# Performance work log

Hardware: AMD Instinct MI355X
Metric: run time of the kernel (lower is better)

The kernel has to match this reference:

```python
import jax, jax.numpy as jnp
import numpy as np

T, B, INPUT, HIDDEN, OUTPUT = 512, 128, 256, 512, 128

def setup_inputs() -> dict:
    key = jax.random.key(0)
    k1, k2, k3 = jax.random.split(key, 3)
    fan_in = INPUT + HIDDEN
    bound = 1.0 / np.sqrt(fan_in)
    x = jax.random.normal(k1, (T, B, INPUT), dtype=jnp.float32)
    W = jax.random.uniform(k2, (HIDDEN, fan_in), minval=-bound, maxval=bound, dtype=jnp.float32)
    b = jax.random.uniform(k3, (HIDDEN,), minval=-bound, maxval=bound, dtype=jnp.float32)
    return {"x": x, "W": W, "b": b}

def reference(x, W, b):
    # W: [H, INPUT+H] (torch Linear layout); split into input and hidden parts
    Wx = W[:, :INPUT]   # [H, I]
    Wh = W[:, INPUT:]   # [H, H]
    h0 = jnp.zeros((x.shape[1], Wh.shape[0]), dtype=x.dtype)
    # precompute input projections for all steps: [T, B, H]
    xp = jnp.einsum('tbi,hi->tbh', x, Wx) + b

    def step(h, xp_t):
        h_new = jnp.tanh(xp_t + h @ Wh.T)
        return h_new, h_new

    _, Hs = jax.lax.scan(step, h0, xp)
    return jnp.concatenate([h0[None], Hs], axis=0)  # [T+1, B, H]
```

## Files before the change

### kernel.cpp

```cpp
#include <hip/hip_runtime.h>
#include <hip/hip_bf16.h>
#include <hip/hip_fp16.h>
#include <stdint.h>

#define T_STEPS 512
#define BATCH   128
#define NIN     256
#define HID     512
#define BH      (BATCH * HID)

typedef _Float16 f16x2 __attribute__((ext_vector_type(2)));
typedef unsigned int u32x4 __attribute__((ext_vector_type(4)));

__device__ __forceinline__ float fdot2u(uint32_t a, uint32_t b, float c) {
#if __has_builtin(__builtin_amdgcn_fdot2)
  return __builtin_amdgcn_fdot2(__builtin_bit_cast(f16x2, a),
                                __builtin_bit_cast(f16x2, b), c, false);
#else
  __half2 ha = __builtin_bit_cast(__half2, a);
  __half2 hb = __builtin_bit_cast(__half2, b);
  return c + __half2float(ha.x) * __half2float(hb.x)
           + __half2float(ha.y) * __half2float(hb.y);
#endif
}

__device__ __forceinline__ float dot8(uint4 w, uint4 x, float a) {
  a = fdot2u(w.x, x.x, a);
  a = fdot2u(w.y, x.y, a);
  a = fdot2u(w.z, x.z, a);
  a = fdot2u(w.w, x.w, a);
  return a;
}

template <int CTRL>
__device__ __forceinline__ float dppadd(float v) {
  int x = __builtin_bit_cast(int, v);
  int y = __builtin_amdgcn_update_dpp(x, x, CTRL, 0xF, 0xF, true);
  return v + __builtin_bit_cast(float, y);
}
__device__ __forceinline__ float red8(float v) {
  v = dppadd<0xB1>(v);
  v = dppadd<0x4E>(v);
  v = dppadd<0x141>(v);
  return v;
}

__global__ void prep_w(const float* __restrict__ W,
                       __half* __restrict__ Wx, __half* __restrict__ Wh,
                       float* __restrict__ io) {
  int idx = blockIdx.x * 256 + threadIdx.x;
  if (idx < BH) io[idx] = 0.f;
  int h = idx / (NIN + HID);
  int c = idx - h * (NIN + HID);
  float v = W[idx];
  if (c < NIN) Wx[h * NIN + c] = __float2half(v);
  else         Wh[h * HID + (c - NIN)] = __float2half(v);
}

__launch_bounds__(256)
__global__ void gemm_xp(const float* __restrict__ x,
                        const __half* __restrict__ Wx,
                        const float* __restrict__ bias,
                        float* __restrict__ xp) {
  __shared__ __align__(16) __half xs[32][256];

  const int bid = blockIdx.x;
  const int m0 = (bid >> 1) * 32;
  const int n0 = (bid & 1) * 256;
  const int tid = threadIdx.x;

  {
    int r = tid >> 3, cb = (tid & 7) * 32;
    const float* src = x + (size_t)(m0 + r) * NIN + cb;
    union { __half h[8]; uint4 u; } cv;
#pragma unroll
    for (int i = 0; i < 4; ++i) {
      float4 f0 = *(const float4*)(src + i * 8);
      float4 f1 = *(const float4*)(src + i * 8 + 4);
      cv.h[0] = __float2half(f0.x); cv.h[1] = __float2half(f0.y);
      cv.h[2] = __float2half(f0.z); cv.h[3] = __float2half(f0.w);
      cv.h[4] = __float2half(f1.x); cv.h[5] = __float2half(f1.y);
      cv.h[6] = __float2half(f1.z); cv.h[7] = __float2half(f1.w);
      *(uint4*)(void*)&xs[r][cb + i * 8] = cv.u;
    }
  }
  __syncthreads();

  const int rg = tid >> 6;
  const int c0 = tid & 63;

  float acc[8][4];
#pragma unroll
  for (int r = 0; r < 8; ++r)
#pragma unroll
    for (int j = 0; j < 4; ++j) acc[r][j] = 0.f;

  for (int kc = 0; kc < NIN; kc += 32) {
    uint4 w[4][4];
#pragma unroll
    for (int j = 0; j < 4; ++j) {
      const __half* wp = Wx + (size_t)(n0 + c0 + 64 * j) * NIN + kc;
#pragma unroll
      for (int i = 0; i < 4; ++i) w[j][i] = *(const uint4*)(wp + i * 8);
    }
#pragma unroll
    for (int r = 0; r < 8; ++r) {
      uint4 xv[4];
#pragma unroll
      for (int i = 0; i < 4; ++i)
        xv[i] = *(const uint4*)(const void*)&xs[rg * 8 + r][kc + i * 8];
#pragma unroll
      for (int j = 0; j < 4; ++j)
#pragma unroll
        for (int i = 0; i < 4; ++i) acc[r][j] = dot8(w[j][i], xv[i], acc[r][j]);
    }
  }

  float bj[4];
#pragma unroll
  for (int j = 0; j < 4; ++j) bj[j] = bias[n0 + c0 + 64 * j];
#pragma unroll
  for (int r = 0; r < 8; ++r) {
    float* dst = xp + (size_t)(m0 + rg * 8 + r) * HID + n0 + c0;
#pragma unroll
    for (int j = 0; j < 4; ++j) dst[64 * j] = acc[r][j] + bj[j];
  }
}

#define HCH 72
__global__ __launch_bounds__(512)
__attribute__((amdgpu_waves_per_eu(2, 2)))
void rnn_scan(const __half* __restrict__ Wh, float* io) {
  __shared__ __align__(16) __half hA[8 * HCH];
  __shared__ __align__(16) __half hB[8 * HCH];

  const int bid  = blockIdx.x;
  const int b    = bid >> 1;
  const int half = bid & 1;
  const int ph0  = (1 - half) * 256;
  const int tid  = threadIdx.x;
  const int ks   = tid & 7;
  const int rb   = tid >> 3;
  const bool em  = (ks < 4);

  uint32_t w[4][32];
  {
    const __half* wrow = Wh + (size_t)(half * 256 + rb * 4) * HID + ks * 64;
#pragma unroll
    for (int r = 0; r < 4; ++r)
#pragma unroll
      for (int i = 0; i < 8; ++i) {
        u32x4 q = *(const u32x4*)(const void*)(wrow + (size_t)r * HID + i * 8);
        w[r][4 * i + 0] = q.x; w[r][4 * i + 1] = q.y;
        w[r][4 * i + 2] = q.z; w[r][4 * i + 3] = q.w;
      }
  }
#pragma unroll
  for (int r = 0; r < 4; ++r)
#pragma unroll
    for (int j = 0; j < 32; ++j)
      asm volatile("" : "+v"(w[r][j]));

  const int myrow = half * 256 + rb * 4 + ks;
  float* iorow = io + (size_t)BH + (size_t)b * HID + myrow;
  const int hwaddr = (myrow >> 6) * HCH + (myrow & 63);
  const int k0 = ph0 + 2 * (tid & 127);
  const int poffw = ((k0 >> 6) * HCH + (k0 & 63)) >> 1;
  const float* pex = io + (size_t)BH + (size_t)b * HID + k0;
  int* flagme = (int*)(io + (size_t)b * HID + half * 256);
  int* flagpt = (int*)(io + (size_t)b * HID + ph0);

  hA[(tid >> 6) * HCH + (tid & 63)] = __float2half(0.f);
  __syncthreads();

  float xpv = em ? *iorow : 0.f;

  auto do_step = [&](const __half* rd, __half* wrb, float xpi, int t) -> float {
    float xpn = 0.f;
    if (em && t + 1 < T_STEPS) xpn = iorow[BH];

    float a0 = 0.f, a1 = 0.f, a2 = 0.f, a3 = 0.f;
    const char* rdp = (const char*)rd + ks * (HCH * 2);
#pragma unroll
    for (int i = 0; i < 8; ++i) {
      u32x4 hj = *(const u32x4*)(const void*)(rdp + i * 16);
      a0 = fdot2u(w[0][4*i+0], hj.x, a0); a0 = fdot2u(w[0][4*i+1], hj.y, a0);
      a0 = fdot2u(w[0][4*i+2], hj.z, a0); a0 = fdot2u(w[0][4*i+3], hj.w, a0);
      a1 = fdot2u(w[1][4*i+0], hj.x, a1); a1 = fdot2u(w[1][4*i+1], hj.y, a1);
      a1 = fdot2u(w[1][4*i+2], hj.z, a1); a1 = fdot2u(w[1][4*i+3], hj.w, a1);
      a2 = fdot2u(w[2][4*i+0], hj.x, a2); a2 = fdot2u(w[2][4*i+1], hj.y, a2);
      a2 = fdot2u(w[2][4*i+2], hj.z, a2); a2 = fdot2u(w[2][4*i+3], hj.w, a2);
      a3 = fdot2u(w[3][4*i+0], hj.x, a3); a3 = fdot2u(w[3][4*i+1], hj.y, a3);
      a3 = fdot2u(w[3][4*i+2], hj.z, a3); a3 = fdot2u(w[3][4*i+3], hj.w, a3);
    }
    a0 = red8(a0); a1 = red8(a1); a2 = red8(a2); a3 = red8(a3);
    float s = (ks == 0) ? a0 : (ks == 1) ? a1 : (ks == 2) ? a2 : a3;

    s += xpi;
    float e  = __expf(fminf(fmaxf(2.f * s, -40.f), 40.f));
    float hn = (e - 1.f) / (e + 1.f);
    if (em) {
      __hip_atomic_store(iorow, hn, __ATOMIC_RELAXED,
                         __HIP_MEMORY_SCOPE_AGENT);
      wrb[hwaddr] = __float2half(hn);
    }
    __syncthreads();

    if (t + 1 < T_STEPS) {
      if (tid == 0) {
        __hip_atomic_store(flagme, t + 1, __ATOMIC_RELAXED,
                           __HIP_MEMORY_SCOPE_AGENT);
        while (__hip_atomic_load(flagpt, __ATOMIC_RELAXED,
                                 __HIP_MEMORY_SCOPE_AGENT) < t + 1) {}
      }
      __syncthreads();
      asm volatile("" ::: "memory");
      if (tid < 128) {
        float f0 = __hip_atomic_load(pex, __ATOMIC_RELAXED,
                                     __HIP_MEMORY_SCOPE_AGENT);
        float f1 = __hip_atomic_load(pex + 1, __ATOMIC_RELAXED,
                                     __HIP_MEMORY_SCOPE_AGENT);
        uint32_t pk =
            (uint32_t)__builtin_bit_cast(unsigned short, __float2half(f0)) |
            ((uint32_t)__builtin_bit_cast(unsigned short, __float2half(f1))
             << 16);
        ((uint32_t*)wrb)[poffw] = pk;
      }
      __syncthreads();
    }
    return xpn;
  };

  for (int t = 0; t < T_STEPS; t += 2) {
    xpv = do_step(hA, hB, xpv, t);
    iorow += BH; pex += BH;
    xpv = do_step(hB, hA, xpv, t + 1);
    iorow += BH; pex += BH;
  }
}

__global__ void zero_flags(float* io) {
  int i = threadIdx.x;
  int b = i >> 1, half = i & 1;
  io[(size_t)b * HID + half * 256] = 0.f;
}

extern "C" void kernel_launch(void* const* d_in, const int* in_sizes, int n_in,
                              void* d_out, int out_size, void* d_ws, size_t ws_size,
                              hipStream_t stream) {
  const float* x    = (const float*)d_in[0];
  const float* W    = (const float*)d_in[1];
  const float* bias = (const float*)d_in[2];

  char* ws = (char*)d_ws;
  __half* Wx = (__half*)ws;
  __half* Wh = (__half*)(ws + 262144);

  float* io = (float*)d_out;
  float* xp = io + (size_t)BH;

  prep_w<<<1536, 256, 0, stream>>>(W, Wx, Wh, io);
  gemm_xp<<<4096, 256, 0, stream>>>(x, Wx, bias, xp);
  rnn_scan<<<256, 512, 0, stream>>>(Wh, io);
  zero_flags<<<1, 256, 0, stream>>>(io);
}
```

Before: 1.348 ms.

## Replace flag handshake with tagged per-element fp16 exchange words in RNN scan

The two blocks that share a batch row used to exchange hidden state through a single flag. Thread 0 set and polled it, followed by two block barriers and fp32 reloads. Now each hidden element is published as one 32-bit word carrying the step tag in the high 16 bits and the fp16 value in the low 16 bits. Consumer threads spin directly on their own word, using two alternating slots so a slot is not overwritten before its reader has taken it. This removes a barrier and the serialized flag round trip from every recurrent step, at the cost of many threads polling global memory at the same time and a scratch area that must be cleared before the scan.

```diff
diff --git a/kernel.cpp b/kernel.cpp
--- a/kernel.cpp
+++ b/kernel.cpp
@@ -127,10 +127,14 @@
   }
 }
 
+__global__ void clear_slot1(uint32_t* ex1) {
+  ex1[blockIdx.x * 256 + threadIdx.x] = 0u;
+}
+
 #define HCH 72
 __global__ __launch_bounds__(512)
 __attribute__((amdgpu_waves_per_eu(2, 2)))
-void rnn_scan(const __half* __restrict__ Wh, float* io) {
+void rnn_scan(const __half* __restrict__ Wh, float* io, uint32_t* ex1) {
   __shared__ __align__(16) __half hA[8 * HCH];
   __shared__ __align__(16) __half hB[8 * HCH];
 
@@ -164,18 +168,20 @@
   const int myrow = half * 256 + rb * 4 + ks;
   float* iorow = io + (size_t)BH + (size_t)b * HID + myrow;
   const int hwaddr = (myrow >> 6) * HCH + (myrow & 63);
-  const int k0 = ph0 + 2 * (tid & 127);
-  const int poffw = ((k0 >> 6) * HCH + (k0 & 63)) >> 1;
-  const float* pex = io + (size_t)BH + (size_t)b * HID + k0;
-  int* flagme = (int*)(io + (size_t)b * HID + half * 256);
-  int* flagpt = (int*)(io + (size_t)b * HID + ph0);
+  uint32_t* exw0 = (uint32_t*)io + (size_t)b * HID + myrow;
+  uint32_t* exw1 = ex1 + (size_t)b * HID + myrow;
+  const uint32_t* exr0 = (uint32_t*)io + (size_t)b * HID + ph0 + tid;
+  const uint32_t* exr1 = ex1 + (size_t)b * HID + ph0 + tid;
+  const int kg = ph0 + tid;
+  const int paddr = (kg >> 6) * HCH + (kg & 63);
 
   hA[(tid >> 6) * HCH + (tid & 63)] = __float2half(0.f);
   __syncthreads();
 
   float xpv = em ? *iorow : 0.f;
 
-  auto do_step = [&](const __half* rd, __half* wrb, float xpi, int t) -> float {
+  auto do_step = [&](const __half* rd, __half* wrb, uint32_t* exw,
+                     const uint32_t* exr, float xpi, int t) -> float {
     float xpn = 0.f;
     if (em && t + 1 < T_STEPS) xpn = iorow[BH];
 
@@ -199,50 +205,44 @@
     s += xpi;
     float e  = __expf(fminf(fmaxf(2.f * s, -40.f), 40.f));
     float hn = (e - 1.f) / (e + 1.f);
+
+    const unsigned short hf16 =
+        __builtin_bit_cast(unsigned short, __float2half(hn));
     if (em) {
-      __hip_atomic_store(iorow, hn, __ATOMIC_RELAXED,
-                         __HIP_MEMORY_SCOPE_AGENT);
-      wrb[hwaddr] = __float2half(hn);
+      *iorow = hn;
+      wrb[hwaddr] = __builtin_bit_cast(__half, hf16);
+    }
+
+    if (t + 1 < T_STEPS) {
+      if (em) {
+        uint32_t word = ((uint32_t)(t + 1) << 16) | (uint32_t)hf16;
+        __hip_atomic_store(exw, word, __ATOMIC_RELAXED,
+                           __HIP_MEMORY_SCOPE_AGENT);
+      }
+      asm volatile("" ::: "memory");
+      if (tid < 256) {
+        uint32_t wv;
+        do {
+          wv = __hip_atomic_load(exr, __ATOMIC_RELAXED,
+                                 __HIP_MEMORY_SCOPE_AGENT);
+        } while ((wv >> 16) != (uint32_t)(t + 1));
+        wrb[paddr] = __builtin_bit_cast(__half, (unsigned short)(wv & 0xFFFF));
+      }
     }
     __syncthreads();
-
-    if (t + 1 < T_STEPS) {
-      if (tid == 0) {
-        __hip_atomic_store(flagme, t + 1, __ATOMIC_RELAXED,
-                           __HIP_MEMORY_SCOPE_AGENT);
-        while (__hip_atomic_load(flagpt, __ATOMIC_RELAXED,
-                                 __HIP_MEMORY_SCOPE_AGENT) < t + 1) {}
-      }
-      __syncthreads();
-      asm volatile("" ::: "memory");
-      if (tid < 128) {
-        float f0 = __hip_atomic_load(pex, __ATOMIC_RELAXED,
-                                     __HIP_MEMORY_SCOPE_AGENT);
-        float f1 = __hip_atomic_load(pex + 1, __ATOMIC_RELAXED,
-                                     __HIP_MEMORY_SCOPE_AGENT);
-        uint32_t pk =
-            (uint32_t)__builtin_bit_cast(unsigned short, __float2half(f0)) |
-            ((uint32_t)__builtin_bit_cast(unsigned short, __float2half(f1))
-             << 16);
-        ((uint32_t*)wrb)[poffw] = pk;
-      }
-      __syncthreads();
-    }
     return xpn;
   };
 
   for (int t = 0; t < T_STEPS; t += 2) {
-    xpv = do_step(hA, hB, xpv, t);
-    iorow += BH; pex += BH;
-    xpv = do_step(hB, hA, xpv, t + 1);
-    iorow += BH; pex += BH;
-  }
-}
-
-__global__ void zero_flags(float* io) {
-  int i = threadIdx.x;
-  int b = i >> 1, half = i & 1;
-  io[(size_t)b * HID + half * 256] = 0.f;
+    xpv = do_step(hA, hB, exw1, exr1, xpv, t);
+    iorow += BH;
+    xpv = do_step(hB, hA, exw0, exr0, xpv, t + 1);
+    iorow += BH;
+  }
+}
+
+__global__ void zero_h0(float* io) {
+  io[blockIdx.x * 256 + threadIdx.x] = 0.f;
 }
 
 extern "C" void kernel_launch(void* const* d_in, const int* in_sizes, int n_in,
@@ -261,6 +261,7 @@
 
   prep_w<<<1536, 256, 0, stream>>>(W, Wx, Wh, io);
   gemm_xp<<<4096, 256, 0, stream>>>(x, Wx, bias, xp);
-  rnn_scan<<<256, 512, 0, stream>>>(Wh, io);
-  zero_flags<<<1, 256, 0, stream>>>(io);
-}
+  clear_slot1<<<256, 256, 0, stream>>>((uint32_t*)ws);
+  rnn_scan<<<256, 512, 0, stream>>>(Wh, io, (uint32_t*)ws);
+  zero_h0<<<256, 256, 0, stream>>>(io);
+}
```

Measured after the change: 1.162 ms. 1.16x faster.
